# Optimization experiments

Measured on AMD Instinct MI355X. Metric: run time of the kernel, lower is better.

Reference implementation:

```python
import jax, jax.numpy as jnp
import numpy as np

C = 256
NUM_HEADS = 8
NUM_GROUPS = 32
EPS = 1e-5


def setup_inputs() -> dict:
    key = jax.random.key(0)
    ks = jax.random.split(key, 7)
    B, H, W = 2, 64, 64
    x = jax.random.normal(ks[0], (B, C, H, W), dtype=jnp.float32)
    norm_gamma = jnp.ones((C,), dtype=jnp.float32)
    norm_beta = jnp.zeros((C,), dtype=jnp.float32)
    # 1x1 convs == per-pixel linear layers; store weights as (out_ch, in_ch)
    qkv_w = jax.random.normal(ks[1], (3 * C, C), dtype=jnp.float32) * (1.0 / np.sqrt(C))
    qkv_b = jnp.zeros((3 * C,), dtype=jnp.float32)
    proj_w = jax.random.normal(ks[2], (C, C), dtype=jnp.float32) * (1.0 / np.sqrt(C))
    proj_b = jnp.zeros((C,), dtype=jnp.float32)
    return {"x": x, "norm_gamma": norm_gamma, "norm_beta": norm_beta,
            "qkv_w": qkv_w, "qkv_b": qkv_b, "proj_w": proj_w, "proj_b": proj_b}


def _group_norm(x, gamma, beta):
    B, Cc, H, W = x.shape
    xg = x.reshape(B, NUM_GROUPS, Cc // NUM_GROUPS, H, W)
    mean = xg.mean(axis=(2, 3, 4), keepdims=True)
    var = xg.var(axis=(2, 3, 4), keepdims=True)
    xn = ((xg - mean) * jax.lax.rsqrt(var + EPS)).reshape(B, Cc, H, W)
    return xn * gamma[None, :, None, None] + beta[None, :, None, None]


def reference(x, norm_gamma, norm_beta, qkv_w, qkv_b, proj_w, proj_b):
    B, Cc, H, W = x.shape
    hd = Cc // NUM_HEADS
    N = H * W

    h = _group_norm(x, norm_gamma, norm_beta)
    # 1x1 conv: (3C,C) x (B,C,H,W) -> (B,3C,H,W)
    qkv = jnp.einsum('oc,bchw->bohw', qkv_w, h) + qkv_b[None, :, None, None]
    q, k, v = jnp.split(qkv, 3, axis=1)

    def heads(t):  # (B,C,H,W) -> (B,heads,N,hd)
        return t.reshape(B, NUM_HEADS, hd, N).transpose(0, 1, 3, 2)

    q, k, v = heads(q), heads(k), heads(v)
    scale = hd ** (-0.5)
    attn = jax.nn.softmax(jnp.einsum('bhnd,bhmd->bhnm', q, k) * scale, axis=-1)
    out = jnp.einsum('bhnm,bhmd->bhnd', attn, v)  # (B,heads,N,hd)
    out = out.transpose(0, 1, 3, 2).reshape(B, Cc, H, W)
    out = jnp.einsum('oc,bchw->bohw', proj_w, out) + proj_b[None, :, None, None]
    return x + out
```

## Files before the change

### kernel.cpp

```cpp
#include <hip/hip_runtime.h>
#include <math.h>

#define C_    256
#define NH    8
#define HD_   32
#define NG    32
#define CPG   8
#define NPIX  4096
#define BATCH 2
#define EPSV  1e-5f
#define SLOG2 0.25503489f
#define MF    16.0f
#define KVB   128
#define KSTR  40
#define VSTR  136
#define KPS2  2048

typedef __bf16 bf16x8 __attribute__((ext_vector_type(8)));
typedef __bf16 bf16x4 __attribute__((ext_vector_type(4)));
typedef float  f32x4  __attribute__((ext_vector_type(4)));

__global__ __launch_bounds__(256) void prep_kernel(const float* __restrict__ x,
                                                   float* __restrict__ stats,
                                                   const float* __restrict__ qw,
                                                   const float* __restrict__ pw,
                                                   __bf16* __restrict__ wbq,
                                                   __bf16* __restrict__ wbp) {
    if (blockIdx.x >= 64) {
        const int i = ((blockIdx.x - 64) * 256 + threadIdx.x) * 4;
        const float* src;
        __bf16* dst;
        int off;
        if (i < 768 * 256) { src = qw; dst = wbq; off = i; }
        else { src = pw; dst = wbp; off = i - 768 * 256; }
        const float4 v = *(const float4*)(src + off);
        bf16x4 o;
        o[0] = (__bf16)v.x; o[1] = (__bf16)v.y; o[2] = (__bf16)v.z; o[3] = (__bf16)v.w;
        *(bf16x4*)(dst + off) = o;
        return;
    }
    const int blk = blockIdx.x;
    const int b = blk >> 5, g = blk & 31;
    const float* __restrict__ xp = x + ((size_t)(b * C_ + g * CPG)) * NPIX;

    float s = 0.f, ss = 0.f;
    for (int i = threadIdx.x * 4; i < CPG * NPIX; i += 256 * 4) {
        const float4 v = *(const float4*)(xp + i);
        s  += v.x + v.y + v.z + v.w;
        ss += v.x * v.x + v.y * v.y + v.z * v.z + v.w * v.w;
    }
    #pragma unroll
    for (int off = 32; off; off >>= 1) {
        s  += __shfl_down(s, off);
        ss += __shfl_down(ss, off);
    }
    __shared__ float ls[4], lss[4];
    const int wid = threadIdx.x >> 6, lane = threadIdx.x & 63;
    if (lane == 0) { ls[wid] = s; lss[wid] = ss; }
    __syncthreads();
    if (threadIdx.x == 0) {
        float S = 0.f, SS = 0.f;
        #pragma unroll
        for (int w = 0; w < 4; ++w) { S += ls[w]; SS += lss[w]; }
        const float inv_n = 1.0f / (float)(CPG * NPIX);
        const float mean = S * inv_n;
        const float var  = SS * inv_n - mean * mean;
        stats[blk * 2 + 0] = mean;
        stats[blk * 2 + 1] = rsqrtf(var + EPSV);
    }
}

__global__ __launch_bounds__(256) void qkv_gemm_kernel(const __bf16* __restrict__ wbq,
                                                       const float* __restrict__ bias,
                                                       const float* __restrict__ x,
                                                       const float* __restrict__ stats,
                                                       const float* __restrict__ gamma,
                                                       const float* __restrict__ beta,
                                                       __bf16* __restrict__ Qb,
                                                       __bf16* __restrict__ Kb,
                                                       __bf16* __restrict__ Vb) {
    const int b = blockIdx.z;
    const int n0 = blockIdx.x * 64;
    __shared__ __align__(16) __bf16 tile[64][264];

    {
        const int nn = (threadIdx.x & 15) * 4;
        #pragma unroll
        for (int p = 0; p < 16; ++p) {
            const int c = (threadIdx.x >> 4) + p * 16;
            const float4 v = *(const float4*)(x + ((size_t)(b * C_ + c)) * NPIX + n0 + nn);
            const int g = c >> 3;
            const float mean = stats[(b * NG + g) * 2 + 0];
            const float rstd = stats[(b * NG + g) * 2 + 1];
            const float ga = gamma[c] * rstd;
            const float be = beta[c] - mean * ga;
            tile[nn + 0][c] = (__bf16)(v.x * ga + be);
            tile[nn + 1][c] = (__bf16)(v.y * ga + be);
            tile[nn + 2][c] = (__bf16)(v.z * ga + be);
            tile[nn + 3][c] = (__bf16)(v.w * ga + be);
        }
    }
    __syncthreads();

    const int wave = threadIdx.x >> 6, lane = threadIdx.x & 63;
    const int col = lane & 15, g = lane >> 4;
    const int m0 = blockIdx.y * 128 + wave * 32;

    f32x4 acc[2][4];
    #pragma unroll
    for (int i = 0; i < 2; ++i)
        #pragma unroll
        for (int j = 0; j < 4; ++j) acc[i][j] = (f32x4){0.f, 0.f, 0.f, 0.f};

    #pragma unroll
    for (int c0 = 0; c0 < C_; c0 += 32) {
        bf16x8 la[2], lb[4];
        #pragma unroll
        for (int mb = 0; mb < 2; ++mb)
            la[mb] = *(const bf16x8*)(wbq + (size_t)(m0 + mb * 16 + col) * C_ + c0 + g * 8);
        #pragma unroll
        for (int nb = 0; nb < 4; ++nb)
            lb[nb] = *(const bf16x8*)(&tile[nb * 16 + col][c0 + g * 8]);
        #pragma unroll
        for (int mb = 0; mb < 2; ++mb)
            #pragma unroll
            for (int nb = 0; nb < 4; ++nb)
                acc[mb][nb] = __builtin_amdgcn_mfma_f32_16x16x32_bf16(la[mb], lb[nb], acc[mb][nb], 0, 0, 0);
    }

    #pragma unroll
    for (int mb = 0; mb < 2; ++mb) {
        const int mbase = m0 + mb * 16 + 4 * g;
        const float4 b4 = *(const float4*)(bias + mbase);
        const int route = mbase >> 8;
        const int bh = b * NH + ((mbase >> 5) & 7);
        const int d0 = mbase & 31;
        #pragma unroll
        for (int nb = 0; nb < 4; ++nb) {
            const int n = n0 + nb * 16 + col;
            f32x4 v = acc[mb][nb];
            v[0] += b4.x; v[1] += b4.y; v[2] += b4.z; v[3] += b4.w;
            if (route == 0) {
                bf16x4 o;
                #pragma unroll
                for (int r = 0; r < 4; ++r) o[r] = (__bf16)(v[r] * SLOG2);
                *(bf16x4*)(Qb + (((size_t)bh * NPIX + n) << 5) + d0) = o;
            } else if (route == 1) {
                bf16x4 o;
                #pragma unroll
                for (int r = 0; r < 4; ++r) o[r] = (__bf16)v[r];
                *(bf16x4*)(Kb + (((size_t)bh * NPIX + n) << 5) + d0) = o;
            } else {
                #pragma unroll
                for (int r = 0; r < 4; ++r)
                    Vb[((size_t)bh * HD_ + d0 + r) * NPIX + n] = (__bf16)v[r];
            }
        }
    }
}

__global__ __launch_bounds__(512) void attn_kernel(const __bf16* __restrict__ Qb,
                                                   const __bf16* __restrict__ Kb,
                                                   const __bf16* __restrict__ Vb,
                                                   __bf16* __restrict__ aot) {
    __shared__ __align__(16) char smem[75776];
    __bf16 (*Ks)[2][KVB][KSTR] = (__bf16 (*)[2][KVB][KSTR])(smem);
    __bf16 (*Vs)[2][HD_][VSTR] = (__bf16 (*)[2][HD_][VSTR])(smem + 40960);
    float* pbuf = (float*)smem;

    const int id = blockIdx.x;
    const int h = id & 7;
    const int rest = id >> 3;
    const int b = rest >> 5;
    const int qt = rest & 31;

    const int wave = threadIdx.x >> 6, lane = threadIdx.x & 63;
    const int hw = wave >> 2, wv = wave & 3;
    const int col = lane & 15, g = lane >> 4;
    const int bh = b * NH + h;
    const int q0 = qt * 128 + wv * 32;

    const __bf16* __restrict__ qp = Qb + ((size_t)bh * NPIX + q0) * HD_;
    const __bf16* __restrict__ kp = Kb + ((size_t)bh * NPIX + hw * KPS2) * HD_;
    const __bf16* __restrict__ vp = Vb + (size_t)bh * HD_ * NPIX + hw * KPS2;

    const int sk_key = wv * 16 + (lane >> 2);
    const int sk_seg = (lane & 3) * 8;
    const int sv_d   = wv * 8 + (lane >> 3);
    const int sv_seg = (lane & 7) * 8;
    const int vslot  = (sv_seg & 32) + ((((sv_seg & 15) >> 2) << 3)) + (((sv_seg >> 4) & 1) << 2);
    const __bf16* __restrict__ kg = kp + (size_t)sk_key * HD_ + sk_seg;
    const __bf16* __restrict__ vg = vp + (size_t)sv_d * NPIX + sv_seg;

    const bf16x8 fq0 = *(const bf16x8*)(qp + col * HD_ + g * 8);
    const bf16x8 fq1 = *(const bf16x8*)(qp + (16 + col) * HD_ + g * 8);

    bf16x8 ones;
    #pragma unroll
    for (int j = 0; j < 8; ++j) ones[j] = (__bf16)1.0f;
    const f32x4 mfc = {-MF, -MF, -MF, -MF};

    f32x4 acc00 = {0.f,0.f,0.f,0.f}, acc01 = {0.f,0.f,0.f,0.f};
    f32x4 acc10 = {0.f,0.f,0.f,0.f}, acc11 = {0.f,0.f,0.f,0.f};
    f32x4 accL0 = {0.f,0.f,0.f,0.f}, accL1 = {0.f,0.f,0.f,0.f};

    {
        const bf16x8 rk0 = *(const bf16x8*)(kg);
        const bf16x8 rk1 = *(const bf16x8*)(kg + (size_t)64 * HD_);
        const bf16x8 rv0 = *(const bf16x8*)(vg);
        const bf16x8 rv1 = *(const bf16x8*)(vg + 64);
        *(bf16x8*)&Ks[hw][0][sk_key][sk_seg]      = rk0;
        *(bf16x8*)&Ks[hw][0][sk_key + 64][sk_seg] = rk1;
        bf16x4 lo, hi;
        #pragma unroll
        for (int j = 0; j < 4; ++j) { lo[j] = rv0[j]; hi[j] = rv0[4 + j]; }
        *(bf16x4*)&Vs[hw][0][sv_d][vslot]     = lo;
        *(bf16x4*)&Vs[hw][0][sv_d][vslot + 8] = hi;
        #pragma unroll
        for (int j = 0; j < 4; ++j) { lo[j] = rv1[j]; hi[j] = rv1[4 + j]; }
        *(bf16x4*)&Vs[hw][0][sv_d][vslot + 64]     = lo;
        *(bf16x4*)&Vs[hw][0][sv_d][vslot + 64 + 8] = hi;
    }
    __syncthreads();

    const int nt = KPS2 / KVB;
    for (int t = 0; t < nt; ++t) {
        const int cur = t & 1;
        bf16x8 nk0, nk1, nv0, nv1;
        const bool more = (t + 1 < nt);
        {
            const size_t koff = (size_t)(more ? (t + 1) * KVB : 0);
            nk0 = *(const bf16x8*)(kg + koff * HD_);
            nk1 = *(const bf16x8*)(kg + (koff + 64) * HD_);
            nv0 = *(const bf16x8*)(vg + koff);
            nv1 = *(const bf16x8*)(vg + koff + 64);
        }

        #pragma unroll
        for (int kk = 0; kk < KVB; kk += 32) {
            const bf16x8 fk0 = *(const bf16x8*)(&Ks[hw][cur][kk + col][g * 8]);
            const bf16x8 fk1 = *(const bf16x8*)(&Ks[hw][cur][kk + 16 + col][g * 8]);
            const bf16x8 fv0 = *(const bf16x8*)(&Vs[hw][cur][col][kk + 8 * g]);
            const bf16x8 fv1 = *(const bf16x8*)(&Vs[hw][cur][col + 16][kk + 8 * g]);

            f32x4 s00 = __builtin_amdgcn_mfma_f32_16x16x32_bf16(fk0, fq0, mfc, 0, 0, 0);
            f32x4 s10 = __builtin_amdgcn_mfma_f32_16x16x32_bf16(fk1, fq0, mfc, 0, 0, 0);
            f32x4 s01 = __builtin_amdgcn_mfma_f32_16x16x32_bf16(fk0, fq1, mfc, 0, 0, 0);
            f32x4 s11 = __builtin_amdgcn_mfma_f32_16x16x32_bf16(fk1, fq1, mfc, 0, 0, 0);

            float p0[8], p1[8];
            #pragma unroll
            for (int r = 0; r < 4; ++r) {
                p0[r]     = __builtin_amdgcn_exp2f(s00[r]);
                p0[4 + r] = __builtin_amdgcn_exp2f(s10[r]);
                p1[r]     = __builtin_amdgcn_exp2f(s01[r]);
                p1[4 + r] = __builtin_amdgcn_exp2f(s11[r]);
            }

            bf16x8 fp0, fp1;
            #pragma unroll
            for (int j = 0; j < 8; ++j) { fp0[j] = (__bf16)p0[j]; fp1[j] = (__bf16)p1[j]; }

            accL0 = __builtin_amdgcn_mfma_f32_16x16x32_bf16(ones, fp0, accL0, 0, 0, 0);
            accL1 = __builtin_amdgcn_mfma_f32_16x16x32_bf16(ones, fp1, accL1, 0, 0, 0);
            acc00 = __builtin_amdgcn_mfma_f32_16x16x32_bf16(fv0, fp0, acc00, 0, 0, 0);
            acc01 = __builtin_amdgcn_mfma_f32_16x16x32_bf16(fv1, fp0, acc01, 0, 0, 0);
            acc10 = __builtin_amdgcn_mfma_f32_16x16x32_bf16(fv0, fp1, acc10, 0, 0, 0);
            acc11 = __builtin_amdgcn_mfma_f32_16x16x32_bf16(fv1, fp1, acc11, 0, 0, 0);
        }

        if (more) {
            *(bf16x8*)&Ks[hw][cur ^ 1][sk_key][sk_seg]      = nk0;
            *(bf16x8*)&Ks[hw][cur ^ 1][sk_key + 64][sk_seg] = nk1;
            bf16x4 lo, hi;
            #pragma unroll
            for (int j = 0; j < 4; ++j) { lo[j] = nv0[j]; hi[j] = nv0[4 + j]; }
            *(bf16x4*)&Vs[hw][cur ^ 1][sv_d][vslot]     = lo;
            *(bf16x4*)&Vs[hw][cur ^ 1][sv_d][vslot + 8] = hi;
            #pragma unroll
            for (int j = 0; j < 4; ++j) { lo[j] = nv1[j]; hi[j] = nv1[4 + j]; }
            *(bf16x4*)&Vs[hw][cur ^ 1][sv_d][vslot + 64]     = lo;
            *(bf16x4*)&Vs[hw][cur ^ 1][sv_d][vslot + 64 + 8] = hi;
        }
        __syncthreads();
    }

    float l0 = accL0[0], l1 = accL1[0];

    if (hw == 1) {
        float* pp = pbuf + ((size_t)wv * 64 + lane) * 20;
        *(f32x4*)(pp + 0)  = acc00;
        *(f32x4*)(pp + 4)  = acc01;
        *(f32x4*)(pp + 8)  = acc10;
        *(f32x4*)(pp + 12) = acc11;
        pp[16] = l0; pp[17] = l1;
    }
    __syncthreads();
    if (hw == 0) {
        const float* pp = pbuf + ((size_t)wv * 64 + lane) * 20;
        const f32x4 b00 = *(const f32x4*)(pp + 0);
        const f32x4 b01 = *(const f32x4*)(pp + 4);
        const f32x4 b10 = *(const f32x4*)(pp + 8);
        const f32x4 b11 = *(const f32x4*)(pp + 12);
        #pragma unroll
        for (int r = 0; r < 4; ++r) {
            acc00[r] += b00[r]; acc01[r] += b01[r];
            acc10[r] += b10[r]; acc11[r] += b11[r];
        }
        const float inv0 = 1.0f / (l0 + pp[16]);
        const float inv1 = 1.0f / (l1 + pp[17]);
        const int cb = h * HD_ + 4 * g;
        {
            __bf16* op = aot + ((size_t)(b * NPIX) + q0 + col) * C_ + cb;
            bf16x4 o0, o1;
            #pragma unroll
            for (int r = 0; r < 4; ++r) { o0[r] = (__bf16)(acc00[r] * inv0); o1[r] = (__bf16)(acc01[r] * inv0); }
            *(bf16x4*)(op) = o0;
            *(bf16x4*)(op + 16) = o1;
        }
        {
            __bf16* op = aot + ((size_t)(b * NPIX) + q0 + 16 + col) * C_ + cb;
            bf16x4 o0, o1;
            #pragma unroll
            for (int r = 0; r < 4; ++r) { o0[r] = (__bf16)(acc10[r] * inv1); o1[r] = (__bf16)(acc11[r] * inv1); }
            *(bf16x4*)(op) = o0;
            *(bf16x4*)(op + 16) = o1;
        }
    }
}

__global__ __launch_bounds__(256) void proj_gemm_kernel(const __bf16* __restrict__ wbp,
                                                        const float* __restrict__ bias,
                                                        const __bf16* __restrict__ aot,
                                                        const float* __restrict__ x,
                                                        float* __restrict__ out) {
    const int b = blockIdx.z;
    const int wave = threadIdx.x >> 6, lane = threadIdx.x & 63;
    const int col = lane & 15, g = lane >> 4;
    const int n0 = blockIdx.x * 64 + (wave & 1) * 32;
    const int m0 = blockIdx.y * 64 + (wave >> 1) * 32;
    const __bf16* __restrict__ ap = aot + (size_t)b * NPIX * C_;

    f32x4 acc[2][2];
    #pragma unroll
    for (int i = 0; i < 2; ++i)
        #pragma unroll
        for (int j = 0; j < 2; ++j) acc[i][j] = (f32x4){0.f, 0.f, 0.f, 0.f};

    #pragma unroll
    for (int c0 = 0; c0 < C_; c0 += 32) {
        bf16x8 la[2], lb[2];
        #pragma unroll
        for (int mb = 0; mb < 2; ++mb)
            la[mb] = *(const bf16x8*)(wbp + (size_t)(m0 + mb * 16 + col) * C_ + c0 + g * 8);
        #pragma unroll
        for (int nb = 0; nb < 2; ++nb)
            lb[nb] = *(const bf16x8*)(ap + (size_t)(n0 + nb * 16 + col) * C_ + c0 + g * 8);
        #pragma unroll
        for (int mb = 0; mb < 2; ++mb)
            #pragma unroll
            for (int nb = 0; nb < 2; ++nb)
                acc[mb][nb] = __builtin_amdgcn_mfma_f32_16x16x32_bf16(la[mb], lb[nb], acc[mb][nb], 0, 0, 0);
    }

    #pragma unroll
    for (int mb = 0; mb < 2; ++mb) {
        const int mbase = m0 + mb * 16 + 4 * g;
        const float4 b4 = *(const float4*)(bias + mbase);
        const float bias_r[4] = {b4.x, b4.y, b4.z, b4.w};
        #pragma unroll
        for (int nb = 0; nb < 2; ++nb) {
            const int n = n0 + nb * 16 + col;
            #pragma unroll
            for (int r = 0; r < 4; ++r) {
                const size_t idx = ((size_t)(b * C_ + mbase + r)) * NPIX + n;
                out[idx] = acc[mb][nb][r] + bias_r[r] + x[idx];
            }
        }
    }
}

extern "C" void kernel_launch(void* const* d_in, const int* in_sizes, int n_in,
                              void* d_out, int out_size, void* d_ws, size_t ws_size,
                              hipStream_t stream) {
    (void)in_sizes; (void)n_in; (void)out_size; (void)ws_size;
    const float* x      = (const float*)d_in[0];
    const float* gamma  = (const float*)d_in[1];
    const float* beta   = (const float*)d_in[2];
    const float* qkv_w  = (const float*)d_in[3];
    const float* qkv_b  = (const float*)d_in[4];
    const float* proj_w = (const float*)d_in[5];
    const float* proj_b = (const float*)d_in[6];
    float* out = (float*)d_out;

    char* ws = (char*)d_ws;
    __bf16* wbq  = (__bf16*)(ws);
    __bf16* wbp  = (__bf16*)(ws + 0x60000);
    float*  stats= (float*) (ws + 0x80000);
    __bf16* Qb   = (__bf16*)(ws + 0x500000);
    __bf16* Kb   = (__bf16*)(ws + 0x900000);
    __bf16* Vb   = (__bf16*)(ws + 0xD00000);
    __bf16* aot  = (__bf16*)(ws + 0x1100000);

    prep_kernel<<<dim3(320), dim3(256), 0, stream>>>(x, stats, qkv_w, proj_w, wbq, wbp);
    qkv_gemm_kernel<<<dim3(NPIX / 64, 768 / 128, BATCH), dim3(256), 0, stream>>>(
        wbq, qkv_b, x, stats, gamma, beta, Qb, Kb, Vb);
    attn_kernel<<<dim3(32 * NH * BATCH), dim3(512), 0, stream>>>(Qb, Kb, Vb, aot);
    proj_gemm_kernel<<<dim3(NPIX / 64, C_ / 64, BATCH), dim3(256), 0, stream>>>(wbp, proj_b, aot, x, out);
}
```

Measured before the change: 84.90 us.

## Store V in MFMA fragment layout and load K/V directly from global in attention

The QKV GEMM now writes V pre-swizzled into the per-lane MFMA operand layout, so the attention kernel can load K and V fragments straight from global/L2 without staging them in LDS or synchronising per tile. Attention blocks shrink to 256 threads covering 32 queries, with four waves splitting the 4096 keys four ways and reducing partial sums through LDS at the end. This removes LDS traffic and barriers but makes each block read K/V from cache repeatedly, with no explicit prefetch or double buffering. The V scatter in the GEMM epilogue also becomes strided 2-byte stores.

```diff
diff --git a/kernel.cpp b/kernel.cpp
--- a/kernel.cpp
+++ b/kernel.cpp
@@ -11,10 +11,7 @@
 #define EPSV  1e-5f
 #define SLOG2 0.25503489f
 #define MF    16.0f
-#define KVB   128
-#define KSTR  40
-#define VSTR  136
-#define KPS2  2048
+#define KPS   1024
 
 typedef __bf16 bf16x8 __attribute__((ext_vector_type(8)));
 typedef __bf16 bf16x4 __attribute__((ext_vector_type(4)));
@@ -78,7 +75,7 @@
                                                        const float* __restrict__ beta,
                                                        __bf16* __restrict__ Qb,
                                                        __bf16* __restrict__ Kb,
-                                                       __bf16* __restrict__ Vb) {
+                                                       __bf16* __restrict__ Vf) {
     const int b = blockIdx.z;
     const int n0 = blockIdx.x * 64;
     __shared__ __align__(16) __bf16 tile[64][264];
@@ -151,46 +148,39 @@
                 for (int r = 0; r < 4; ++r) o[r] = (__bf16)v[r];
                 *(bf16x4*)(Kb + (((size_t)bh * NPIX + n) << 5) + d0) = o;
             } else {
+                const int j = n & 31;
+                const int gj = (j & 15) >> 2;
+                const int s = (j & 3) + ((j >> 4) << 2);
+                __bf16* vfb = Vf + (((size_t)(bh * 128 + (n >> 5)) * 2 + (d0 >> 4)) << 9) + s;
                 #pragma unroll
                 for (int r = 0; r < 4; ++r)
-                    Vb[((size_t)bh * HD_ + d0 + r) * NPIX + n] = (__bf16)v[r];
+                    vfb[(((d0 & 15) + r) + 16 * gj) * 8] = (__bf16)v[r];
             }
         }
     }
 }
 
-__global__ __launch_bounds__(512) void attn_kernel(const __bf16* __restrict__ Qb,
+__global__ __launch_bounds__(256) void attn_kernel(const __bf16* __restrict__ Qb,
                                                    const __bf16* __restrict__ Kb,
-                                                   const __bf16* __restrict__ Vb,
+                                                   const __bf16* __restrict__ Vf,
                                                    __bf16* __restrict__ aot) {
-    __shared__ __align__(16) char smem[75776];
-    __bf16 (*Ks)[2][KVB][KSTR] = (__bf16 (*)[2][KVB][KSTR])(smem);
-    __bf16 (*Vs)[2][HD_][VSTR] = (__bf16 (*)[2][HD_][VSTR])(smem + 40960);
-    float* pbuf = (float*)smem;
+    __shared__ __align__(16) float pbuf[4 * 64 * 20];
 
     const int id = blockIdx.x;
     const int h = id & 7;
-    const int rest = id >> 3;
-    const int b = rest >> 5;
-    const int qt = rest & 31;
-
-    const int wave = threadIdx.x >> 6, lane = threadIdx.x & 63;
-    const int hw = wave >> 2, wv = wave & 3;
+    const int b = (id >> 3) & 1;
+    const int qt = id >> 4;
+
+    const int sp = threadIdx.x >> 6;
+    const int lane = threadIdx.x & 63;
     const int col = lane & 15, g = lane >> 4;
     const int bh = b * NH + h;
-    const int q0 = qt * 128 + wv * 32;
+    const int q0 = qt * 32;
 
     const __bf16* __restrict__ qp = Qb + ((size_t)bh * NPIX + q0) * HD_;
-    const __bf16* __restrict__ kp = Kb + ((size_t)bh * NPIX + hw * KPS2) * HD_;
-    const __bf16* __restrict__ vp = Vb + (size_t)bh * HD_ * NPIX + hw * KPS2;
-
-    const int sk_key = wv * 16 + (lane >> 2);
-    const int sk_seg = (lane & 3) * 8;
-    const int sv_d   = wv * 8 + (lane >> 3);
-    const int sv_seg = (lane & 7) * 8;
-    const int vslot  = (sv_seg & 32) + ((((sv_seg & 15) >> 2) << 3)) + (((sv_seg >> 4) & 1) << 2);
-    const __bf16* __restrict__ kg = kp + (size_t)sk_key * HD_ + sk_seg;
-    const __bf16* __restrict__ vg = vp + (size_t)sv_d * NPIX + sv_seg;
+    const __bf16* __restrict__ kg0 = Kb + ((size_t)bh * NPIX + sp * KPS + col) * HD_ + g * 8;
+    const __bf16* __restrict__ kg1 = kg0 + 16 * HD_;
+    const __bf16* __restrict__ vfp = Vf + (((size_t)(bh * 128 + sp * 32) * 2) << 9) + lane * 8;
 
     const bf16x8 fq0 = *(const bf16x8*)(qp + col * HD_ + g * 8);
     const bf16x8 fq1 = *(const bf16x8*)(qp + (16 + col) * HD_ + g * 8);
@@ -204,111 +194,66 @@
     f32x4 acc10 = {0.f,0.f,0.f,0.f}, acc11 = {0.f,0.f,0.f,0.f};
     f32x4 accL0 = {0.f,0.f,0.f,0.f}, accL1 = {0.f,0.f,0.f,0.f};
 
+    #pragma unroll 2
+    for (int t = 0; t < KPS / 32; ++t) {
+        const bf16x8 fk0 = *(const bf16x8*)(kg0 + (size_t)t * 32 * HD_);
+        const bf16x8 fk1 = *(const bf16x8*)(kg1 + (size_t)t * 32 * HD_);
+        const bf16x8 fv0 = *(const bf16x8*)(vfp + t * 1024);
+        const bf16x8 fv1 = *(const bf16x8*)(vfp + t * 1024 + 512);
+
+        f32x4 s00 = __builtin_amdgcn_mfma_f32_16x16x32_bf16(fk0, fq0, mfc, 0, 0, 0);
+        f32x4 s10 = __builtin_amdgcn_mfma_f32_16x16x32_bf16(fk1, fq0, mfc, 0, 0, 0);
+        f32x4 s01 = __builtin_amdgcn_mfma_f32_16x16x32_bf16(fk0, fq1, mfc, 0, 0, 0);
+        f32x4 s11 = __builtin_amdgcn_mfma_f32_16x16x32_bf16(fk1, fq1, mfc, 0, 0, 0);
+
+        float p0[8], p1[8];
+        #pragma unroll
+        for (int r = 0; r < 4; ++r) {
+            p0[r]     = __builtin_amdgcn_exp2f(s00[r]);
+            p0[4 + r] = __builtin_amdgcn_exp2f(s10[r]);
+            p1[r]     = __builtin_amdgcn_exp2f(s01[r]);
+            p1[4 + r] = __builtin_amdgcn_exp2f(s11[r]);
+        }
+
+        bf16x8 fp0, fp1;
+        #pragma unroll
+        for (int j = 0; j < 8; ++j) { fp0[j] = (__bf16)p0[j]; fp1[j] = (__bf16)p1[j]; }
+
+        accL0 = __builtin_amdgcn_mfma_f32_16x16x32_bf16(ones, fp0, accL0, 0, 0, 0);
+        accL1 = __builtin_amdgcn_mfma_f32_16x16x32_bf16(ones, fp1, accL1, 0, 0, 0);
+        acc00 = __builtin_amdgcn_mfma_f32_16x16x32_bf16(fv0, fp0, acc00, 0, 0, 0);
+        acc01 = __builtin_amdgcn_mfma_f32_16x16x32_bf16(fv1, fp0, acc01, 0, 0, 0);
+        acc10 = __builtin_amdgcn_mfma_f32_16x16x32_bf16(fv0, fp1, acc10, 0, 0, 0);
+        acc11 = __builtin_amdgcn_mfma_f32_16x16x32_bf16(fv1, fp1, acc11, 0, 0, 0);
+    }
+
     {
-        const bf16x8 rk0 = *(const bf16x8*)(kg);
-        const bf16x8 rk1 = *(const bf16x8*)(kg + (size_t)64 * HD_);
-        const bf16x8 rv0 = *(const bf16x8*)(vg);
-        const bf16x8 rv1 = *(const bf16x8*)(vg + 64);
-        *(bf16x8*)&Ks[hw][0][sk_key][sk_seg]      = rk0;
-        *(bf16x8*)&Ks[hw][0][sk_key + 64][sk_seg] = rk1;
-        bf16x4 lo, hi;
-        #pragma unroll
-        for (int j = 0; j < 4; ++j) { lo[j] = rv0[j]; hi[j] = rv0[4 + j]; }
-        *(bf16x4*)&Vs[hw][0][sv_d][vslot]     = lo;
-        *(bf16x4*)&Vs[hw][0][sv_d][vslot + 8] = hi;
-        #pragma unroll
-        for (int j = 0; j < 4; ++j) { lo[j] = rv1[j]; hi[j] = rv1[4 + j]; }
-        *(bf16x4*)&Vs[hw][0][sv_d][vslot + 64]     = lo;
-        *(bf16x4*)&Vs[hw][0][sv_d][vslot + 64 + 8] = hi;
-    }
-    __syncthreads();
-
-    const int nt = KPS2 / KVB;
-    for (int t = 0; t < nt; ++t) {
-        const int cur = t & 1;
-        bf16x8 nk0, nk1, nv0, nv1;
-        const bool more = (t + 1 < nt);
-        {
-            const size_t koff = (size_t)(more ? (t + 1) * KVB : 0);
-            nk0 = *(const bf16x8*)(kg + koff * HD_);
-            nk1 = *(const bf16x8*)(kg + (koff + 64) * HD_);
-            nv0 = *(const bf16x8*)(vg + koff);
-            nv1 = *(const bf16x8*)(vg + koff + 64);
-        }
-
-        #pragma unroll
-        for (int kk = 0; kk < KVB; kk += 32) {
-            const bf16x8 fk0 = *(const bf16x8*)(&Ks[hw][cur][kk + col][g * 8]);
-            const bf16x8 fk1 = *(const bf16x8*)(&Ks[hw][cur][kk + 16 + col][g * 8]);
-            const bf16x8 fv0 = *(const bf16x8*)(&Vs[hw][cur][col][kk + 8 * g]);
-            const bf16x8 fv1 = *(const bf16x8*)(&Vs[hw][cur][col + 16][kk + 8 * g]);
-
-            f32x4 s00 = __builtin_amdgcn_mfma_f32_16x16x32_bf16(fk0, fq0, mfc, 0, 0, 0);
-            f32x4 s10 = __builtin_amdgcn_mfma_f32_16x16x32_bf16(fk1, fq0, mfc, 0, 0, 0);
-            f32x4 s01 = __builtin_amdgcn_mfma_f32_16x16x32_bf16(fk0, fq1, mfc, 0, 0, 0);
-            f32x4 s11 = __builtin_amdgcn_mfma_f32_16x16x32_bf16(fk1, fq1, mfc, 0, 0, 0);
-
-            float p0[8], p1[8];
-            #pragma unroll
-            for (int r = 0; r < 4; ++r) {
-                p0[r]     = __builtin_amdgcn_exp2f(s00[r]);
-                p0[4 + r] = __builtin_amdgcn_exp2f(s10[r]);
-                p1[r]     = __builtin_amdgcn_exp2f(s01[r]);
-                p1[4 + r] = __builtin_amdgcn_exp2f(s11[r]);
-            }
-
-            bf16x8 fp0, fp1;
-            #pragma unroll
-            for (int j = 0; j < 8; ++j) { fp0[j] = (__bf16)p0[j]; fp1[j] = (__bf16)p1[j]; }
-
-            accL0 = __builtin_amdgcn_mfma_f32_16x16x32_bf16(ones, fp0, accL0, 0, 0, 0);
-            accL1 = __builtin_amdgcn_mfma_f32_16x16x32_bf16(ones, fp1, accL1, 0, 0, 0);
-            acc00 = __builtin_amdgcn_mfma_f32_16x16x32_bf16(fv0, fp0, acc00, 0, 0, 0);
-            acc01 = __builtin_amdgcn_mfma_f32_16x16x32_bf16(fv1, fp0, acc01, 0, 0, 0);
-            acc10 = __builtin_amdgcn_mfma_f32_16x16x32_bf16(fv0, fp1, acc10, 0, 0, 0);
-            acc11 = __builtin_amdgcn_mfma_f32_16x16x32_bf16(fv1, fp1, acc11, 0, 0, 0);
-        }
-
-        if (more) {
-            *(bf16x8*)&Ks[hw][cur ^ 1][sk_key][sk_seg]      = nk0;
-            *(bf16x8*)&Ks[hw][cur ^ 1][sk_key + 64][sk_seg] = nk1;
-            bf16x4 lo, hi;
-            #pragma unroll
-            for (int j = 0; j < 4; ++j) { lo[j] = nv0[j]; hi[j] = nv0[4 + j]; }
-            *(bf16x4*)&Vs[hw][cur ^ 1][sv_d][vslot]     = lo;
-            *(bf16x4*)&Vs[hw][cur ^ 1][sv_d][vslot + 8] = hi;
-            #pragma unroll
-            for (int j = 0; j < 4; ++j) { lo[j] = nv1[j]; hi[j] = nv1[4 + j]; }
-            *(bf16x4*)&Vs[hw][cur ^ 1][sv_d][vslot + 64]     = lo;
-            *(bf16x4*)&Vs[hw][cur ^ 1][sv_d][vslot + 64 + 8] = hi;
-        }
-        __syncthreads();
-    }
-
-    float l0 = accL0[0], l1 = accL1[0];
-
-    if (hw == 1) {
-        float* pp = pbuf + ((size_t)wv * 64 + lane) * 20;
+        float* pp = pbuf + ((size_t)sp * 64 + lane) * 20;
         *(f32x4*)(pp + 0)  = acc00;
         *(f32x4*)(pp + 4)  = acc01;
         *(f32x4*)(pp + 8)  = acc10;
         *(f32x4*)(pp + 12) = acc11;
-        pp[16] = l0; pp[17] = l1;
+        pp[16] = accL0[0]; pp[17] = accL1[0];
     }
     __syncthreads();
-    if (hw == 0) {
-        const float* pp = pbuf + ((size_t)wv * 64 + lane) * 20;
-        const f32x4 b00 = *(const f32x4*)(pp + 0);
-        const f32x4 b01 = *(const f32x4*)(pp + 4);
-        const f32x4 b10 = *(const f32x4*)(pp + 8);
-        const f32x4 b11 = *(const f32x4*)(pp + 12);
-        #pragma unroll
-        for (int r = 0; r < 4; ++r) {
-            acc00[r] += b00[r]; acc01[r] += b01[r];
-            acc10[r] += b10[r]; acc11[r] += b11[r];
-        }
-        const float inv0 = 1.0f / (l0 + pp[16]);
-        const float inv1 = 1.0f / (l1 + pp[17]);
+    if (sp == 0) {
+        float l0 = accL0[0], l1 = accL1[0];
+        #pragma unroll
+        for (int s = 1; s < 4; ++s) {
+            const float* pp = pbuf + ((size_t)s * 64 + lane) * 20;
+            const f32x4 b00 = *(const f32x4*)(pp + 0);
+            const f32x4 b01 = *(const f32x4*)(pp + 4);
+            const f32x4 b10 = *(const f32x4*)(pp + 8);
+            const f32x4 b11 = *(const f32x4*)(pp + 12);
+            #pragma unroll
+            for (int r = 0; r < 4; ++r) {
+                acc00[r] += b00[r]; acc01[r] += b01[r];
+                acc10[r] += b10[r]; acc11[r] += b11[r];
+            }
+            l0 += pp[16]; l1 += pp[17];
+        }
+        const float inv0 = 1.0f / l0;
+        const float inv1 = 1.0f / l1;
         const int cb = h * HD_ + 4 * g;
         {
             __bf16* op = aot + ((size_t)(b * NPIX) + q0 + col) * C_ + cb;
@@ -399,12 +344,12 @@
     float*  stats= (float*) (ws + 0x80000);
     __bf16* Qb   = (__bf16*)(ws + 0x500000);
     __bf16* Kb   = (__bf16*)(ws + 0x900000);
-    __bf16* Vb   = (__bf16*)(ws + 0xD00000);
+    __bf16* Vf   = (__bf16*)(ws + 0xD00000);
     __bf16* aot  = (__bf16*)(ws + 0x1100000);
 
     prep_kernel<<<dim3(320), dim3(256), 0, stream>>>(x, stats, qkv_w, proj_w, wbq, wbp);
     qkv_gemm_kernel<<<dim3(NPIX / 64, 768 / 128, BATCH), dim3(256), 0, stream>>>(
-        wbq, qkv_b, x, stats, gamma, beta, Qb, Kb, Vb);
-    attn_kernel<<<dim3(32 * NH * BATCH), dim3(512), 0, stream>>>(Qb, Kb, Vb, aot);
+        wbq, qkv_b, x, stats, gamma, beta, Qb, Kb, Vf);
+    attn_kernel<<<dim3(128 * NH * BATCH), dim3(256), 0, stream>>>(Qb, Kb, Vf, aot);
     proj_gemm_kernel<<<dim3(NPIX / 64, C_ / 64, BATCH), dim3(256), 0, stream>>>(wbp, proj_b, aot, x, out);
 }
```

New measurement: 96.07 us. +13.2%, slower.
